# Performance work log

Measured on AMD Instinct MI355X. Metric: run time of the kernel, lower is better.

Reference implementation:

```python
import jax, jax.numpy as jnp
import numpy as np
from jax import lax

B, N, NPOINT, NSAMPLE = 16, 8192, 2048, 32
RADIUS = 0.45
D_FEAT = 64
MLP = (64, 64, 128)
EPS = 1e-5  # BatchNorm2d default eps


def setup_inputs() -> dict:
    key = jax.random.key(0)
    ks = jax.random.split(key, 8)
    inp = {
        "xyz": jax.random.uniform(ks[0], (B, 3, N), dtype=jnp.float32),
        "points": jax.random.normal(ks[1], (B, D_FEAT, N), dtype=jnp.float32),
    }
    dims = (3 + D_FEAT,) + MLP
    for i in range(len(MLP)):
        ci, co = dims[i], dims[i + 1]
        inp[f"W{i}"] = jax.random.normal(ks[2 + i], (co, ci), dtype=jnp.float32) / np.float32(np.sqrt(ci))
        inp[f"b{i}"] = jnp.zeros((co,), jnp.float32)
        inp[f"gamma{i}"] = jnp.ones((co,), jnp.float32)
        inp[f"beta{i}"] = jnp.zeros((co,), jnp.float32)
    return inp


def _fps(xyz_t, npoint):
    # farthest point sampling; xyz_t: [B, N, 3] -> [B, npoint] indices
    Bc, Nc, _ = xyz_t.shape

    def step(carry, _):
        distance, farthest = carry
        centroid = jnp.take_along_axis(xyz_t, farthest[:, None, None], axis=1)  # [B,1,3]
        d = jnp.sum((xyz_t - centroid) ** 2, axis=-1)  # [B,N]
        distance = jnp.minimum(distance, d)
        return (distance, jnp.argmax(distance, axis=-1)), farthest

    init = (jnp.full((Bc, Nc), 1e10, xyz_t.dtype), jnp.zeros((Bc,), jnp.int32))
    _, cents = lax.scan(step, init, None, length=npoint)
    return jnp.transpose(cents)  # [B, npoint]


def _gather(pts, idx):
    # pts: [B, N, C], idx: [B, ...] -> [B, ..., C]
    return jax.vmap(lambda p, i: p[i])(pts, idx)


def _forward(xyz, points, params):
    xyz_t = jnp.transpose(xyz, (0, 2, 1))     # [B,N,3]
    pts_t = jnp.transpose(points, (0, 2, 1))  # [B,N,D]

    fps_idx = _fps(xyz_t, NPOINT)
    new_xyz = _gather(xyz_t, fps_idx)         # [B,S,3]

    # ball query -- faithful to source: Euclidean DISTANCE compared vs radius**2
    d2 = (jnp.sum(new_xyz ** 2, -1)[:, :, None]
          + jnp.sum(xyz_t ** 2, -1)[:, None, :]
          - 2.0 * jnp.einsum('bsc,bnc->bsn', new_xyz, xyz_t))
    dist = jnp.sqrt(jnp.maximum(d2, 0.0))     # [B,S,N] == torch.cdist
    neg_vals, idx = lax.top_k(-dist, NSAMPLE)
    group_idx = jnp.where(-neg_vals < RADIUS ** 2, idx, 0)  # [B,S,K]

    grouped_xyz = _gather(xyz_t, group_idx) - new_xyz[:, :, None, :]  # [B,S,K,3]
    grouped_pts = _gather(pts_t, group_idx)                           # [B,S,K,D]
    feats = jnp.concatenate([grouped_xyz, grouped_pts], axis=-1)      # [B,S,K,3+D]

    # shared MLP: 1x1 conv + BatchNorm (training-mode batch stats) + ReLU
    for (W, b, g, be) in params:
        h = jnp.einsum('bskc,oc->bsko', feats, W) + b
        mean = jnp.mean(h, axis=(0, 1, 2))
        var = jnp.var(h, axis=(0, 1, 2))  # biased, like torch BN normalization
        feats = jax.nn.relu(g * (h - mean) * lax.rsqrt(var + EPS) + be)

    new_points = jnp.max(feats, axis=2)  # max over nsample -> [B,S,C_out]
    return jnp.transpose(new_xyz, (0, 2, 1)), jnp.transpose(new_points, (0, 2, 1))


def reference(xyz, points, W0, b0, gamma0, beta0, W1, b1, gamma1, beta1, W2, b2, gamma2, beta2):
    params = [(W0, b0, gamma0, beta0), (W1, b1, gamma1, beta1), (W2, b2, gamma2, beta2)]
    return _forward(xyz, points, params)
```

## Files before the change

### kernel.cpp

```cpp
#include <hip/hip_runtime.h>

#define B_ 16
#define N_ 8192
#define S_ 2048
#define K_ 32
#define EPSBN 1e-5
#define CAP 1024

#define OFF_PARTA    0ul
#define OFF_NEWXYZ   131072ul
#define OFF_GIDX     524288ul
#define OFF_Q1       4718592ul
#define OFF_C1       38273024ul
#define OFF_PART     46661632ul
#define OFF_AFF1     55050240ul
#define OFF_AFF2     55051264ul
#define OFF_AFF3     55052288ul
#define OFF_H3MAX    55053312ul
#define OFF_H3MIN    71830528ul
#define OFF_H2       88607744ul
#define WS_NEED_H2   (OFF_H2 + 268435456ul)

#define STG(row, c) ((row)*33 + ((row)>>5) + (c))

template<int CTRL, int RM>
__device__ __forceinline__ unsigned long long dppmove(unsigned long long x) {
    unsigned int lo = (unsigned int)x, hi = (unsigned int)(x >> 32);
    unsigned int lo2 = (unsigned int)__builtin_amdgcn_update_dpp((int)lo, (int)lo, CTRL, RM, 0xf, false);
    unsigned int hi2 = (unsigned int)__builtin_amdgcn_update_dpp((int)hi, (int)hi, CTRL, RM, 0xf, false);
    return ((unsigned long long)hi2 << 32) | lo2;
}
__device__ __forceinline__ unsigned long long wave_max_u64(unsigned long long x) {
    unsigned long long t;
    t = dppmove<0x111, 0xf>(x); x = (t > x) ? t : x;
    t = dppmove<0x112, 0xf>(x); x = (t > x) ? t : x;
    t = dppmove<0x114, 0xf>(x); x = (t > x) ? t : x;
    t = dppmove<0x118, 0xf>(x); x = (t > x) ? t : x;
    t = dppmove<0x142, 0xa>(x); x = (t > x) ? t : x;
    t = dppmove<0x143, 0xc>(x); x = (t > x) ? t : x;
    return x;
}
__device__ __forceinline__ unsigned long long wave_min_u64(unsigned long long x) {
    unsigned long long t;
    t = dppmove<0x111, 0xf>(x); x = (t < x) ? t : x;
    t = dppmove<0x112, 0xf>(x); x = (t < x) ? t : x;
    t = dppmove<0x114, 0xf>(x); x = (t < x) ? t : x;
    t = dppmove<0x118, 0xf>(x); x = (t < x) ? t : x;
    t = dppmove<0x142, 0xa>(x); x = (t < x) ? t : x;
    t = dppmove<0x143, 0xc>(x); x = (t < x) ? t : x;
    return x;
}

__global__ __launch_bounds__(512) void fps_kernel(const float* __restrict__ xyz,
                                                  const float* __restrict__ pts,
                                                  const float* __restrict__ W0,
                                                  const float* __restrict__ b0,
                                                  float* __restrict__ Q1,
                                                  float* __restrict__ nxyz,
                                                  float* __restrict__ out0) {
    __shared__ float xs[N_], ys[N_], zs[N_];
    __shared__ int farHist[S_];
    __shared__ unsigned long long kq[2][4];
    int tid = threadIdx.x;
    if (blockIdx.x >= 16) {
        int o = tid & 63, jj = tid >> 6;
        int blk = blockIdx.x - 16;
        int b = blk >> 10;
        int j = ((blk & 1023) << 3) + jj;
        const float* xb = xyz + (size_t)b * 3 * N_;
        const float* pb = pts + (size_t)b * 64 * N_;
        float acc = b0[o];
#pragma unroll
        for (int c = 0; c < 3; c++) acc += W0[o * 67 + c] * xb[c * N_ + j];
#pragma unroll 8
        for (int c = 0; c < 64; c++) acc += W0[o * 67 + 3 + c] * pb[c * N_ + j];
        Q1[(((size_t)b << 13) + j) * 64 + o] = acc;
        return;
    }
    int b = blockIdx.x;
    const float* xb = xyz + (size_t)b * 3 * N_;
    for (int i = tid; i < N_; i += 512) {
        xs[i] = xb[i]; ys[i] = xb[N_ + i]; zs[i] = xb[2 * N_ + i];
    }
    __syncthreads();
    float px[32], py[32], pz[32], d8[32];
    if (tid < 256) {
#pragma unroll
        for (int k = 0; k < 32; k++) {
            int i = tid + k * 256;
            px[k] = xs[i]; py[k] = ys[i]; pz[k] = zs[i];
            d8[k] = 1e10f;
        }
    }
    int far = 0;
    int w = tid >> 6;
    for (int t = 0; t < S_; t++) {
        if (tid < 256) {
            if (tid == 0) farHist[t] = far;
            float cx = xs[far], cy = ys[far], cz = zs[far];
            float bv = -1.f; int bk = 0;
#pragma unroll
            for (int k = 0; k < 32; k++) {
                float dx = px[k] - cx, dy = py[k] - cy, dz = pz[k] - cz;
                float d = dx * dx + dy * dy + dz * dz;
                float dd = fminf(d8[k], d); d8[k] = dd;
                if (dd > bv) { bv = dd; bk = k; }
            }
            int bi = tid + bk * 256;
            unsigned long long kk = (((unsigned long long)__float_as_uint(bv)) << 32)
                                  | (unsigned)(8191 - bi);
            kk = wave_max_u64(kk);
            if ((tid & 63) == 63) kq[t & 1][w] = kk;
        }
        __syncthreads();
        if (tid < 256) {
            int buf = t & 1;
            unsigned long long fk = kq[buf][0];
#pragma unroll
            for (int q = 1; q < 4; q++) { unsigned long long o = kq[buf][q]; fk = (o > fk) ? o : fk; }
            far = 8191 - (int)(fk & 0xffffffffull);
        }
    }
    __syncthreads();
    for (int s = tid; s < S_; s += 512) {
        int idx = farHist[s];
        float x = xs[idx], y = ys[idx], z = zs[idx];
        int g = b * S_ + s;
        nxyz[g * 3 + 0] = x; nxyz[g * 3 + 1] = y; nxyz[g * 3 + 2] = z;
        out0[(b * 3 + 0) * S_ + s] = x;
        out0[(b * 3 + 1) * S_ + s] = y;
        out0[(b * 3 + 2) * S_ + s] = z;
    }
}

__global__ __launch_bounds__(64) void ball_kernel(const float* __restrict__ xyz,
                                                  const float* __restrict__ nxyz,
                                                  int* __restrict__ gidx) {
    __shared__ unsigned long long keys[CAP];
    __shared__ int cnt;
    int bs = blockIdx.x; int b = bs >> 11; int tid = threadIdx.x;
    const float* xb = xyz + (size_t)b * 3 * N_;
    float cx = nxyz[bs * 3 + 0], cy = nxyz[bs * 3 + 1], cz = nxyz[bs * 3 + 2];
    float csq = __fadd_rn(__fadd_rn(__fmul_rn(cx, cx), __fmul_rn(cy, cy)), __fmul_rn(cz, cz));
    const float R2F = (float)(0.45 * 0.45);
    if (tid == 0) cnt = 0;
    __syncthreads();
    for (int j = tid; j < N_; j += 64) {
        float qx = xb[j], qy = xb[N_ + j], qz = xb[2 * N_ + j];
        float psq = __fadd_rn(__fadd_rn(__fmul_rn(qx, qx), __fmul_rn(qy, qy)), __fmul_rn(qz, qz));
        float t = __fmul_rn(cx, qx);
        t = __fmaf_rn(cy, qy, t);
        t = __fmaf_rn(cz, qz, t);
        float d2 = __fsub_rn(__fadd_rn(csq, psq), __fadd_rn(t, t));
        float dist = __fsqrt_rn(fmaxf(d2, 0.0f));
        if (dist < R2F) {
            int p = atomicAdd(&cnt, 1);
            if (p < CAP) keys[p] = (((unsigned long long)__float_as_uint(dist)) << 32) | (unsigned)j;
        }
    }
    __syncthreads();
    int nc = cnt; if (nc > CAP) nc = CAP;
    for (int k = 0; k < K_; k++) {
        unsigned long long bk = ~0ull;
        for (int i = tid; i < nc; i += 64) {
            unsigned long long kv = keys[i];
            bk = (kv < bk) ? kv : bk;
        }
        bk = wave_min_u64(bk);
        unsigned int lo = (unsigned int)__builtin_amdgcn_readlane((int)(unsigned int)bk, 63);
        unsigned int hi = (unsigned int)__builtin_amdgcn_readlane((int)(unsigned int)(bk >> 32), 63);
        unsigned long long mk = ((unsigned long long)hi << 32) | lo;
        int j = 0;
        if (mk != ~0ull) {
            j = (int)(mk & 0xffffffffull);
            for (int i = tid; i < nc; i += 64)
                if (keys[i] == mk) keys[i] = ~0ull;
        }
        if (tid == 0) gidx[bs * K_ + k] = j;
    }
}

__global__ __launch_bounds__(256) void c1_kernel(const float* __restrict__ nxyz,
                                                 const float* __restrict__ W0,
                                                 float* __restrict__ C1) {
    int tid = threadIdx.x; int o = tid & 63, ss = tid >> 6;
    int gs = blockIdx.x * 4 + ss;
    float acc = 0.f;
#pragma unroll
    for (int c = 0; c < 3; c++) acc += W0[o * 67 + c] * nxyz[gs * 3 + c];
    C1[(size_t)gs * 64 + o] = acc;
}

__global__ __launch_bounds__(256) void stats1_kernel(const float* __restrict__ Q1,
                                                     const float* __restrict__ C1,
                                                     const int* __restrict__ gidx,
                                                     double* __restrict__ part) {
    __shared__ double ds1[4][64], ds2[4][64];
    int tid = threadIdx.x; int o = tid & 63, ll = tid >> 6;
    double s1 = 0, s2 = 0;
    for (int it = 0; it < 256; it++) {
        int slot = it * 4096 + blockIdx.x * 4 + ll;
        int b = slot >> 16; int r = slot & 65535; int s = r >> 5;
        int g = gidx[slot];
        float q = Q1[(((size_t)b << 13) + g) * 64 + o];
        float c = C1[((size_t)(b << 11) + s) * 64 + o];
        float h = q - c;
        s1 += h; s2 += (double)h * (double)h;
    }
    ds1[ll][o] = s1; ds2[ll][o] = s2;
    __syncthreads();
    if (tid < 64) {
        double a = 0, bb = 0;
        for (int l = 0; l < 4; l++) { a += ds1[l][tid]; bb += ds2[l][tid]; }
        part[blockIdx.x * 256 + tid * 2] = a;
        part[blockIdx.x * 256 + tid * 2 + 1] = bb;
    }
}

__global__ void stats_reduceA_kernel(const double* __restrict__ part, int nblocks,
                                     double* __restrict__ partA) {
    int per = nblocks >> 6;
    int a = blockIdx.x;
    int c = threadIdx.x;
    double s = 0;
    for (int k = 0; k < per; k++)
        s += part[((size_t)(a * per + k)) * 256 + c];
    partA[(size_t)a * 256 + c] = s;
}

__global__ void stats_reduce_kernel(const double* __restrict__ part, int nblocks, int C,
                                    const float* __restrict__ gamma, const float* __restrict__ beta,
                                    float* __restrict__ aff) {
    __shared__ double s1s[512], s2s[512];
    int tid = threadIdx.x;
    int q = tid / C; int o = tid - q * C;
    double s1 = 0, s2 = 0;
    for (int i = q; i < nblocks; i += 4) {
        s1 += part[(size_t)i * 256 + o * 2];
        s2 += part[(size_t)i * 256 + o * 2 + 1];
    }
    s1s[tid] = s1; s2s[tid] = s2;
    __syncthreads();
    if (tid < C) {
        double a1 = s1s[tid] + s1s[tid + C] + s1s[tid + 2 * C] + s1s[tid + 3 * C];
        double a2 = s2s[tid] + s2s[tid + C] + s2s[tid + 2 * C] + s2s[tid + 3 * C];
        const double cnt = 1048576.0;
        double mean = a1 / cnt;
        double var = a2 / cnt - mean * mean; if (var < 0) var = 0;
        double a = (double)gamma[tid] / sqrt(var + EPSBN);
        double c = (double)beta[tid] - a * mean;
        aff[tid] = (float)a; aff[C + tid] = (float)c;
    }
}

__global__ __launch_bounds__(256) void layer2_stats_kernel(const float* __restrict__ Q1,
                                                           const float* __restrict__ C1,
                                                           const int* __restrict__ gidx,
                                                           const float* __restrict__ aff1,
                                                           const float* __restrict__ W1,
                                                           const float* __restrict__ b1,
                                                           double* __restrict__ part,
                                                           float* __restrict__ h2out) {
    __shared__ __align__(16) float Wl[64 * 64];
    __shared__ float stage[256 * 33 + 8];
    __shared__ float sA[64], sC[64], sB[64];
    __shared__ double r1[8][33], r2[8][33];
    int tid = threadIdx.x;
    for (int i = tid; i < 4096; i += 256) { int o = i >> 6, c = i & 63; Wl[c * 64 + o] = W1[i]; }
    if (tid < 64) { sA[tid] = aff1[tid]; sC[tid] = aff1[64 + tid]; sB[tid] = b1[tid]; }
    __syncthreads();
    int slot = blockIdx.x * 256 + tid;
    int b = slot >> 16; int r = slot & 65535; int s = r >> 5;
    int g = gidx[slot];
    float x[64];
    {
        const float4* qp4 = (const float4*)(Q1 + (((size_t)b << 13) + g) * 64);
        const float4* cp4 = (const float4*)(C1 + ((size_t)(b << 11) + s) * 64);
#pragma unroll
        for (int c4 = 0; c4 < 16; c4++) {
            float4 q = qp4[c4], cc = cp4[c4];
            int c = c4 * 4;
            x[c + 0] = fmaxf(0.f, sA[c + 0] * (q.x - cc.x) + sC[c + 0]);
            x[c + 1] = fmaxf(0.f, sA[c + 1] * (q.y - cc.y) + sC[c + 1]);
            x[c + 2] = fmaxf(0.f, sA[c + 2] * (q.z - cc.z) + sC[c + 2]);
            x[c + 3] = fmaxf(0.f, sA[c + 3] * (q.w - cc.w) + sC[c + 3]);
        }
    }
    const float4* Wl4 = (const float4*)Wl;
    for (int ch = 0; ch < 2; ch++) {
        float acc[32];
#pragma unroll
        for (int o = 0; o < 32; o++) acc[o] = sB[ch * 32 + o];
#pragma unroll
        for (int c = 0; c < 64; c++) {
            float xv = x[c];
#pragma unroll
            for (int og = 0; og < 8; og++) {
                float4 w = Wl4[c * 16 + ch * 8 + og];
                acc[og * 4 + 0] += w.x * xv; acc[og * 4 + 1] += w.y * xv;
                acc[og * 4 + 2] += w.z * xv; acc[og * 4 + 3] += w.w * xv;
            }
        }
        if (h2out) {
            float4* o4 = (float4*)(h2out + (size_t)slot * 64 + ch * 32);
#pragma unroll
            for (int og = 0; og < 8; og++)
                o4[og] = make_float4(acc[og * 4 + 0], acc[og * 4 + 1], acc[og * 4 + 2], acc[og * 4 + 3]);
        }
#pragma unroll
        for (int o = 0; o < 32; o++) stage[STG(tid, o)] = acc[o];
        __syncthreads();
        int chn = tid & 31, rr = tid >> 5;
        double s1 = 0, s2 = 0;
        for (int row = rr * 32; row < rr * 32 + 32; row++) {
            float v = stage[STG(row, chn)];
            s1 += v; s2 += (double)v * (double)v;
        }
        r1[rr][chn] = s1; r2[rr][chn] = s2;
        __syncthreads();
        if (tid < 32) {
            double a = 0, bb = 0;
            for (int l = 0; l < 8; l++) { a += r1[l][tid]; bb += r2[l][tid]; }
            part[blockIdx.x * 256 + (ch * 32 + tid) * 2] = a;
            part[blockIdx.x * 256 + (ch * 32 + tid) * 2 + 1] = bb;
        }
        __syncthreads();
    }
}

__global__ __launch_bounds__(256) void layer3_kernel(const float* __restrict__ Q1,
                                                     const float* __restrict__ C1,
                                                     const int* __restrict__ gidx,
                                                     const float* __restrict__ aff1,
                                                     const float* __restrict__ aff2,
                                                     const float* __restrict__ W1,
                                                     const float* __restrict__ b1,
                                                     const float* __restrict__ W2,
                                                     const float* __restrict__ b2,
                                                     double* __restrict__ part,
                                                     float* __restrict__ h3max,
                                                     float* __restrict__ h3min) {
    __shared__ __align__(16) float Wl[64 * 128];
    __shared__ float stage[256 * 33 + 8];
    __shared__ float sA1[64], sC1[64], sB1[64], sA2[64], sC2[64], sB2[128];
    __shared__ double r1[8][33], r2[8][33];
    int tid = threadIdx.x;
    for (int i = tid; i < 4096; i += 256) { int o = i >> 6, c = i & 63; Wl[c * 64 + o] = W1[i]; }
    if (tid < 64) {
        sA1[tid] = aff1[tid]; sC1[tid] = aff1[64 + tid]; sB1[tid] = b1[tid];
        sA2[tid] = aff2[tid]; sC2[tid] = aff2[64 + tid];
    }
    __syncthreads();
    int slot = blockIdx.x * 256 + tid;
    int b = slot >> 16; int r = slot & 65535; int s = r >> 5;
    int g = gidx[slot];
    float x[64];
    {
        const float4* qp4 = (const float4*)(Q1 + (((size_t)b << 13) + g) * 64);
        const float4* cp4 = (const float4*)(C1 + ((size_t)(b << 11) + s) * 64);
#pragma unroll
        for (int c4 = 0; c4 < 16; c4++) {
            float4 q = qp4[c4], cc = cp4[c4];
            int c = c4 * 4;
            x[c + 0] = fmaxf(0.f, sA1[c + 0] * (q.x - cc.x) + sC1[c + 0]);
            x[c + 1] = fmaxf(0.f, sA1[c + 1] * (q.y - cc.y) + sC1[c + 1]);
            x[c + 2] = fmaxf(0.f, sA1[c + 2] * (q.z - cc.z) + sC1[c + 2]);
            x[c + 3] = fmaxf(0.f, sA1[c + 3] * (q.w - cc.w) + sC1[c + 3]);
        }
    }
    const float4* Wl4 = (const float4*)Wl;
    float x3[64];
    for (int ch = 0; ch < 2; ch++) {
        float acc[32];
#pragma unroll
        for (int o = 0; o < 32; o++) acc[o] = sB1[ch * 32 + o];
#pragma unroll
        for (int c = 0; c < 64; c++) {
            float xv = x[c];
#pragma unroll
            for (int og = 0; og < 8; og++) {
                float4 w = Wl4[c * 16 + ch * 8 + og];
                acc[og * 4 + 0] += w.x * xv; acc[og * 4 + 1] += w.y * xv;
                acc[og * 4 + 2] += w.z * xv; acc[og * 4 + 3] += w.w * xv;
            }
        }
#pragma unroll
        for (int o = 0; o < 32; o++) {
            int oo = ch * 32 + o;
            x3[oo] = fmaxf(0.f, sA2[oo] * acc[o] + sC2[oo]);
        }
    }
    __syncthreads();
    for (int i = tid; i < 8192; i += 256) { int o = i >> 6, c = i & 63; Wl[c * 128 + o] = W2[i]; }
    if (tid < 128) sB2[tid] = b2[tid];
    __syncthreads();
    for (int ch = 0; ch < 4; ch++) {
        float acc[32];
#pragma unroll
        for (int o = 0; o < 32; o++) acc[o] = sB2[ch * 32 + o];
#pragma unroll
        for (int c = 0; c < 64; c++) {
            float xv = x3[c];
#pragma unroll
            for (int og = 0; og < 8; og++) {
                float4 w = Wl4[c * 32 + ch * 8 + og];
                acc[og * 4 + 0] += w.x * xv; acc[og * 4 + 1] += w.y * xv;
                acc[og * 4 + 2] += w.z * xv; acc[og * 4 + 3] += w.w * xv;
            }
        }
#pragma unroll
        for (int o = 0; o < 32; o++) stage[STG(tid, o)] = acc[o];
        __syncthreads();
        int chn = tid & 31, rr = tid >> 5;
        double s1 = 0, s2 = 0;
        float mx = -3.402823466e38f, mn = 3.402823466e38f;
        for (int row = rr * 32; row < rr * 32 + 32; row++) {
            float v = stage[STG(row, chn)];
            s1 += v; s2 += (double)v * (double)v;
            mx = fmaxf(mx, v); mn = fminf(mn, v);
        }
        r1[rr][chn] = s1; r2[rr][chn] = s2;
        int gg = blockIdx.x * 8 + rr;
        int bb_ = gg >> 11, ss_ = gg & 2047;
        h3max[((size_t)bb_ * 128 + ch * 32 + chn) * 2048 + ss_] = mx;
        h3min[((size_t)bb_ * 128 + ch * 32 + chn) * 2048 + ss_] = mn;
        __syncthreads();
        if (tid < 32) {
            double a = 0, bb = 0;
            for (int l = 0; l < 8; l++) { a += r1[l][tid]; bb += r2[l][tid]; }
            part[blockIdx.x * 256 + (ch * 32 + tid) * 2] = a;
            part[blockIdx.x * 256 + (ch * 32 + tid) * 2 + 1] = bb;
        }
        __syncthreads();
    }
}

__global__ __launch_bounds__(256) void layer3_fast_kernel(const float* __restrict__ h2in,
                                                          const float* __restrict__ aff2,
                                                          const float* __restrict__ W2,
                                                          const float* __restrict__ b2,
                                                          double* __restrict__ part,
                                                          float* __restrict__ h3max,
                                                          float* __restrict__ h3min) {
    __shared__ __align__(16) float Wl[64 * 128];
    __shared__ float stage[256 * 33 + 8];
    __shared__ float sA2[64], sC2[64], sB2[128];
    __shared__ double r1[8][33], r2[8][33];
    int tid = threadIdx.x;
    for (int i = tid; i < 8192; i += 256) { int o = i >> 6, c = i & 63; Wl[c * 128 + o] = W2[i]; }
    if (tid < 64) { sA2[tid] = aff2[tid]; sC2[tid] = aff2[64 + tid]; }
    if (tid < 128) sB2[tid] = b2[tid];
    __syncthreads();
    int slot = blockIdx.x * 256 + tid;
    float x3[64];
    {
        const float4* h4 = (const float4*)(h2in + (size_t)slot * 64);
#pragma unroll
        for (int c4 = 0; c4 < 16; c4++) {
            float4 h = h4[c4];
            int c = c4 * 4;
            x3[c + 0] = fmaxf(0.f, sA2[c + 0] * h.x + sC2[c + 0]);
            x3[c + 1] = fmaxf(0.f, sA2[c + 1] * h.y + sC2[c + 1]);
            x3[c + 2] = fmaxf(0.f, sA2[c + 2] * h.z + sC2[c + 2]);
            x3[c + 3] = fmaxf(0.f, sA2[c + 3] * h.w + sC2[c + 3]);
        }
    }
    const float4* Wl4 = (const float4*)Wl;
    for (int ch = 0; ch < 4; ch++) {
        float acc[32];
#pragma unroll
        for (int o = 0; o < 32; o++) acc[o] = sB2[ch * 32 + o];
#pragma unroll
        for (int c = 0; c < 64; c++) {
            float xv = x3[c];
#pragma unroll
            for (int og = 0; og < 8; og++) {
                float4 w = Wl4[c * 32 + ch * 8 + og];
                acc[og * 4 + 0] += w.x * xv; acc[og * 4 + 1] += w.y * xv;
                acc[og * 4 + 2] += w.z * xv; acc[og * 4 + 3] += w.w * xv;
            }
        }
#pragma unroll
        for (int o = 0; o < 32; o++) stage[STG(tid, o)] = acc[o];
        __syncthreads();
        int chn = tid & 31, rr = tid >> 5;
        double s1 = 0, s2 = 0;
        float mx = -3.402823466e38f, mn = 3.402823466e38f;
        for (int row = rr * 32; row < rr * 32 + 32; row++) {
            float v = stage[STG(row, chn)];
            s1 += v; s2 += (double)v * (double)v;
            mx = fmaxf(mx, v); mn = fminf(mn, v);
        }
        r1[rr][chn] = s1; r2[rr][chn] = s2;
        int gg = blockIdx.x * 8 + rr;
        int bb_ = gg >> 11, ss_ = gg & 2047;
        h3max[((size_t)bb_ * 128 + ch * 32 + chn) * 2048 + ss_] = mx;
        h3min[((size_t)bb_ * 128 + ch * 32 + chn) * 2048 + ss_] = mn;
        __syncthreads();
        if (tid < 32) {
            double a = 0, bb = 0;
            for (int l = 0; l < 8; l++) { a += r1[l][tid]; bb += r2[l][tid]; }
            part[blockIdx.x * 256 + (ch * 32 + tid) * 2] = a;
            part[blockIdx.x * 256 + (ch * 32 + tid) * 2 + 1] = bb;
        }
        __syncthreads();
    }
}

__global__ void final_kernel(const float* __restrict__ h3max, const float* __restrict__ h3min,
                             const float* __restrict__ aff3, float* __restrict__ out1) {
    int idx = blockIdx.x * 256 + threadIdx.x;
    int ch = (idx >> 11) & 127;
    float a = aff3[ch], cv = aff3[128 + ch];
    float v = (a >= 0.f) ? h3max[idx] : h3min[idx];
    out1[idx] = fmaxf(0.f, a * v + cv);
}

extern "C" void kernel_launch(void* const* d_in, const int* in_sizes, int n_in,
                              void* d_out, int out_size, void* d_ws, size_t ws_size,
                              hipStream_t stream) {
    (void)in_sizes; (void)n_in; (void)out_size;
    const float* xyz = (const float*)d_in[0];
    const float* pts = (const float*)d_in[1];
    const float* W0  = (const float*)d_in[2];
    const float* b0  = (const float*)d_in[3];
    const float* g0  = (const float*)d_in[4];
    const float* be0 = (const float*)d_in[5];
    const float* W1  = (const float*)d_in[6];
    const float* b1  = (const float*)d_in[7];
    const float* g1  = (const float*)d_in[8];
    const float* be1 = (const float*)d_in[9];
    const float* W2  = (const float*)d_in[10];
    const float* b2  = (const float*)d_in[11];
    const float* g2  = (const float*)d_in[12];
    const float* be2 = (const float*)d_in[13];

    char* ws = (char*)d_ws;
    double* partA  = (double*)(ws + OFF_PARTA);
    float*  nxyz   = (float*)(ws + OFF_NEWXYZ);
    int*    gidx   = (int*)(ws + OFF_GIDX);
    float*  Q1     = (float*)(ws + OFF_Q1);
    float*  C1b    = (float*)(ws + OFF_C1);
    double* part   = (double*)(ws + OFF_PART);
    float*  aff1   = (float*)(ws + OFF_AFF1);
    float*  aff2   = (float*)(ws + OFF_AFF2);
    float*  aff3   = (float*)(ws + OFF_AFF3);
    float*  h3mx   = (float*)(ws + OFF_H3MAX);
    float*  h3mn   = (float*)(ws + OFF_H3MIN);
    float*  out0   = (float*)d_out;
    float*  out1   = out0 + B_ * 3 * S_;

    bool useH2 = ws_size >= WS_NEED_H2;
    float* h2buf = useH2 ? (float*)(ws + OFF_H2) : (float*)0;

    fps_kernel<<<16 + 16384, 512, 0, stream>>>(xyz, pts, W0, b0, Q1, nxyz, out0);
    ball_kernel<<<B_ * S_, 64, 0, stream>>>(xyz, nxyz, gidx);
    c1_kernel<<<(B_ * S_) / 4, 256, 0, stream>>>(nxyz, W0, C1b);
    stats1_kernel<<<1024, 256, 0, stream>>>(Q1, C1b, gidx, part);
    stats_reduceA_kernel<<<64, 256, 0, stream>>>(part, 1024, partA);
    stats_reduce_kernel<<<1, 256, 0, stream>>>(partA, 64, 64, g0, be0, aff1);
    layer2_stats_kernel<<<4096, 256, 0, stream>>>(Q1, C1b, gidx, aff1, W1, b1, part, h2buf);
    stats_reduceA_kernel<<<64, 256, 0, stream>>>(part, 4096, partA);
    stats_reduce_kernel<<<1, 256, 0, stream>>>(partA, 64, 64, g1, be1, aff2);
    if (useH2) {
        layer3_fast_kernel<<<4096, 256, 0, stream>>>(h2buf, aff2, W2, b2, part, h3mx, h3mn);
    } else {
        layer3_kernel<<<4096, 256, 0, stream>>>(Q1, C1b, gidx, aff1, aff2, W1, b1, W2, b2,
                                                part, h3mx, h3mn);
    }
    stats_reduceA_kernel<<<64, 256, 0, stream>>>(part, 4096, partA);
    stats_reduce_kernel<<<1, 512, 0, stream>>>(partA, 64, 128, g2, be2, aff3);
    final_kernel<<<(B_ * 128 * S_) / 256, 256, 0, stream>>>(h3mx, h3mn, aff3, out1);
}
```

Baseline: 3.591 ms.

## Store layer-2 intermediate in fp16 and coalesce per-group max/min writes

```diff
diff --git a/kernel.cpp b/kernel.cpp
--- a/kernel.cpp
+++ b/kernel.cpp
@@ -1,4 +1,5 @@
 #include <hip/hip_runtime.h>
+#include <hip/hip_fp16.h>
 
 #define B_ 16
 #define N_ 8192
@@ -19,7 +20,7 @@
 #define OFF_H3MAX    55053312ul
 #define OFF_H3MIN    71830528ul
 #define OFF_H2       88607744ul
-#define WS_NEED_H2   (OFF_H2 + 268435456ul)
+#define WS_NEED_H2   (OFF_H2 + 134217728ul)
 
 #define STG(row, c) ((row)*33 + ((row)>>5) + (c))
 
@@ -259,8 +260,7 @@
                                                            const float* __restrict__ aff1,
                                                            const float* __restrict__ W1,
                                                            const float* __restrict__ b1,
-                                                           double* __restrict__ part,
-                                                           float* __restrict__ h2out) {
+                                                           double* __restrict__ part) {
     __shared__ __align__(16) float Wl[64 * 64];
     __shared__ float stage[256 * 33 + 8];
     __shared__ float sA[64], sC[64], sB[64];
@@ -301,11 +301,80 @@
                 acc[og * 4 + 2] += w.z * xv; acc[og * 4 + 3] += w.w * xv;
             }
         }
-        if (h2out) {
-            float4* o4 = (float4*)(h2out + (size_t)slot * 64 + ch * 32);
-#pragma unroll
-            for (int og = 0; og < 8; og++)
-                o4[og] = make_float4(acc[og * 4 + 0], acc[og * 4 + 1], acc[og * 4 + 2], acc[og * 4 + 3]);
+#pragma unroll
+        for (int o = 0; o < 32; o++) stage[STG(tid, o)] = acc[o];
+        __syncthreads();
+        int chn = tid & 31, rr = tid >> 5;
+        double s1 = 0, s2 = 0;
+        for (int row = rr * 32; row < rr * 32 + 32; row++) {
+            float v = stage[STG(row, chn)];
+            s1 += v; s2 += (double)v * (double)v;
+        }
+        r1[rr][chn] = s1; r2[rr][chn] = s2;
+        __syncthreads();
+        if (tid < 32) {
+            double a = 0, bb = 0;
+            for (int l = 0; l < 8; l++) { a += r1[l][tid]; bb += r2[l][tid]; }
+            part[blockIdx.x * 256 + (ch * 32 + tid) * 2] = a;
+            part[blockIdx.x * 256 + (ch * 32 + tid) * 2 + 1] = bb;
+        }
+        __syncthreads();
+    }
+}
+
+__global__ __launch_bounds__(256) void layer2_stats_store_kernel(const float* __restrict__ Q1,
+                                                                 const float* __restrict__ C1,
+                                                                 const int* __restrict__ gidx,
+                                                                 const float* __restrict__ aff1,
+                                                                 const float* __restrict__ W1,
+                                                                 const float* __restrict__ b1,
+                                                                 double* __restrict__ part,
+                                                                 __half* __restrict__ h2out) {
+    __shared__ __align__(16) float Wl[64 * 64];
+    __shared__ float stage[256 * 33 + 8];
+    __shared__ float sA[64], sC[64], sB[64];
+    __shared__ double r1[8][33], r2[8][33];
+    int tid = threadIdx.x;
+    for (int i = tid; i < 4096; i += 256) { int o = i >> 6, c = i & 63; Wl[c * 64 + o] = W1[i]; }
+    if (tid < 64) { sA[tid] = aff1[tid]; sC[tid] = aff1[64 + tid]; sB[tid] = b1[tid]; }
+    __syncthreads();
+    int slot = blockIdx.x * 256 + tid;
+    int b = slot >> 16; int r = slot & 65535; int s = r >> 5;
+    int g = gidx[slot];
+    float x[64];
+    {
+        const float4* qp4 = (const float4*)(Q1 + (((size_t)b << 13) + g) * 64);
+        const float4* cp4 = (const float4*)(C1 + ((size_t)(b << 11) + s) * 64);
+#pragma unroll
+        for (int c4 = 0; c4 < 16; c4++) {
+            float4 q = qp4[c4], cc = cp4[c4];
+            int c = c4 * 4;
+            x[c + 0] = fmaxf(0.f, sA[c + 0] * (q.x - cc.x) + sC[c + 0]);
+            x[c + 1] = fmaxf(0.f, sA[c + 1] * (q.y - cc.y) + sC[c + 1]);
+            x[c + 2] = fmaxf(0.f, sA[c + 2] * (q.z - cc.z) + sC[c + 2]);
+            x[c + 3] = fmaxf(0.f, sA[c + 3] * (q.w - cc.w) + sC[c + 3]);
+        }
+    }
+    const float4* Wl4 = (const float4*)Wl;
+    for (int ch = 0; ch < 2; ch++) {
+        float acc[32];
+#pragma unroll
+        for (int o = 0; o < 32; o++) acc[o] = sB[ch * 32 + o];
+#pragma unroll
+        for (int c = 0; c < 64; c++) {
+            float xv = x[c];
+#pragma unroll
+            for (int og = 0; og < 8; og++) {
+                float4 w = Wl4[c * 16 + ch * 8 + og];
+                acc[og * 4 + 0] += w.x * xv; acc[og * 4 + 1] += w.y * xv;
+                acc[og * 4 + 2] += w.z * xv; acc[og * 4 + 3] += w.w * xv;
+            }
+        }
+        {
+            __half2* o2 = (__half2*)(h2out + ((size_t)slot * 64 + ch * 32));
+#pragma unroll
+            for (int i = 0; i < 16; i++)
+                o2[i] = __floats2half2_rn(acc[2 * i], acc[2 * i + 1]);
         }
 #pragma unroll
         for (int o = 0; o < 32; o++) stage[STG(tid, o)] = acc[o];
@@ -421,9 +490,8 @@
         }
         r1[rr][chn] = s1; r2[rr][chn] = s2;
         int gg = blockIdx.x * 8 + rr;
-        int bb_ = gg >> 11, ss_ = gg & 2047;
-        h3max[((size_t)bb_ * 128 + ch * 32 + chn) * 2048 + ss_] = mx;
-        h3min[((size_t)bb_ * 128 + ch * 32 + chn) * 2048 + ss_] = mn;
+        h3max[(size_t)gg * 128 + ch * 32 + chn] = mx;
+        h3min[(size_t)gg * 128 + ch * 32 + chn] = mn;
         __syncthreads();
         if (tid < 32) {
             double a = 0, bb = 0;
@@ -435,7 +503,7 @@
     }
 }
 
-__global__ __launch_bounds__(256) void layer3_fast_kernel(const float* __restrict__ h2in,
+__global__ __launch_bounds__(256) void layer3_fast_kernel(const __half* __restrict__ h2in,
                                                           const float* __restrict__ aff2,
                                                           const float* __restrict__ W2,
                                                           const float* __restrict__ b2,
@@ -454,15 +522,13 @@
     int slot = blockIdx.x * 256 + tid;
     float x3[64];
     {
-        const float4* h4 = (const float4*)(h2in + (size_t)slot * 64);
-#pragma unroll
-        for (int c4 = 0; c4 < 16; c4++) {
-            float4 h = h4[c4];
-            int c = c4 * 4;
-            x3[c + 0] = fmaxf(0.f, sA2[c + 0] * h.x + sC2[c + 0]);
-            x3[c + 1] = fmaxf(0.f, sA2[c + 1] * h.y + sC2[c + 1]);
-            x3[c + 2] = fmaxf(0.f, sA2[c + 2] * h.z + sC2[c + 2]);
-            x3[c + 3] = fmaxf(0.f, sA2[c + 3] * h.w + sC2[c + 3]);
+        const __half2* hp = (const __half2*)(h2in + (size_t)slot * 64);
+#pragma unroll
+        for (int c2 = 0; c2 < 32; c2++) {
+            float2 f = __half22float2(hp[c2]);
+            int c = c2 * 2;
+            x3[c + 0] = fmaxf(0.f, sA2[c + 0] * f.x + sC2[c + 0]);
+            x3[c + 1] = fmaxf(0.f, sA2[c + 1] * f.y + sC2[c + 1]);
         }
     }
     const float4* Wl4 = (const float4*)Wl;
@@ -493,9 +559,8 @@
         }
         r1[rr][chn] = s1; r2[rr][chn] = s2;
         int gg = blockIdx.x * 8 + rr;
-        int bb_ = gg >> 11, ss_ = gg & 2047;
-        h3max[((size_t)bb_ * 128 + ch * 32 + chn) * 2048 + ss_] = mx;
-        h3min[((size_t)bb_ * 128 + ch * 32 + chn) * 2048 + ss_] = mn;
+        h3max[(size_t)gg * 128 + ch * 32 + chn] = mx;
+        h3min[(size_t)gg * 128 + ch * 32 + chn] = mn;
         __syncthreads();
         if (tid < 32) {
             double a = 0, bb = 0;
@@ -507,13 +572,33 @@
     }
 }
 
-__global__ void final_kernel(const float* __restrict__ h3max, const float* __restrict__ h3min,
-                             const float* __restrict__ aff3, float* __restrict__ out1) {
-    int idx = blockIdx.x * 256 + threadIdx.x;
-    int ch = (idx >> 11) & 127;
-    float a = aff3[ch], cv = aff3[128 + ch];
-    float v = (a >= 0.f) ? h3max[idx] : h3min[idx];
-    out1[idx] = fmaxf(0.f, a * v + cv);
+__global__ __launch_bounds__(256) void final_kernel(const float* __restrict__ h3max,
+                                                    const float* __restrict__ h3min,
+                                                    const float* __restrict__ aff3,
+                                                    float* __restrict__ out1) {
+    __shared__ float tmx[128][17], tmn[128][17];
+    __shared__ float sA3[128], sC3[128];
+    int tid = threadIdx.x;
+    int gg0 = blockIdx.x * 16;
+    if (tid < 128) { sA3[tid] = aff3[tid]; sC3[tid] = aff3[128 + tid]; }
+#pragma unroll
+    for (int e = 0; e < 8; e++) {
+        int t = e * 256 + tid;
+        int gl = t >> 7, c = t & 127;
+        tmx[c][gl] = h3max[(size_t)gg0 * 128 + t];
+        tmn[c][gl] = h3min[(size_t)gg0 * 128 + t];
+    }
+    __syncthreads();
+    int b = gg0 >> 11;
+    int ss0 = gg0 & 2047;
+#pragma unroll
+    for (int e = 0; e < 8; e++) {
+        int t = e * 256 + tid;
+        int c = t >> 4, gl = t & 15;
+        float a = sA3[c], cv = sC3[c];
+        float v = (a >= 0.f) ? tmx[c][gl] : tmn[c][gl];
+        out1[((size_t)b * 128 + c) * 2048 + ss0 + gl] = fmaxf(0.f, a * v + cv);
+    }
 }
 
 extern "C" void kernel_launch(void* const* d_in, const int* in_sizes, int n_in,
@@ -551,7 +636,7 @@
     float*  out1   = out0 + B_ * 3 * S_;
 
     bool useH2 = ws_size >= WS_NEED_H2;
-    float* h2buf = useH2 ? (float*)(ws + OFF_H2) : (float*)0;
+    __half* h2buf = useH2 ? (__half*)(ws + OFF_H2) : (__half*)0;
 
     fps_kernel<<<16 + 16384, 512, 0, stream>>>(xyz, pts, W0, b0, Q1, nxyz, out0);
     ball_kernel<<<B_ * S_, 64, 0, stream>>>(xyz, nxyz, gidx);
@@ -559,7 +644,11 @@
     stats1_kernel<<<1024, 256, 0, stream>>>(Q1, C1b, gidx, part);
     stats_reduceA_kernel<<<64, 256, 0, stream>>>(part, 1024, partA);
     stats_reduce_kernel<<<1, 256, 0, stream>>>(partA, 64, 64, g0, be0, aff1);
-    layer2_stats_kernel<<<4096, 256, 0, stream>>>(Q1, C1b, gidx, aff1, W1, b1, part, h2buf);
+    if (useH2) {
+        layer2_stats_store_kernel<<<4096, 256, 0, stream>>>(Q1, C1b, gidx, aff1, W1, b1, part, h2buf);
+    } else {
+        layer2_stats_kernel<<<4096, 256, 0, stream>>>(Q1, C1b, gidx, aff1, W1, b1, part);
+    }
     stats_reduceA_kernel<<<64, 256, 0, stream>>>(part, 4096, partA);
     stats_reduce_kernel<<<1, 256, 0, stream>>>(partA, 64, 64, g1, be1, aff2);
     if (useH2) {
@@ -570,5 +659,5 @@
     }
     stats_reduceA_kernel<<<64, 256, 0, stream>>>(part, 4096, partA);
     stats_reduce_kernel<<<1, 512, 0, stream>>>(partA, 64, 128, g2, be2, aff3);
-    final_kernel<<<(B_ * 128 * S_) / 256, 256, 0, stream>>>(h3mx, h3mn, aff3, out1);
-}
+    final_kernel<<<(B_ * S_) / 16, 256, 0, stream>>>(h3mx, h3mn, aff3, out1);
+}
```

Measured after the change: 3.209 ms. -10.7%, faster.
